# Optimization experiments

Hardware: AMD Instinct MI355X
Metric: run time of the kernel (lower is better)

The kernel has to match this reference:

```python
import jax, jax.numpy as jnp
import numpy as np

H = 1024        # hidden_size
F = 4096        # intermediate_size
E = 8           # num_local_experts
TOP_K = 2       # num_experts_per_tok
B, S = 1, 2048


def setup_inputs() -> dict:
    key = jax.random.key(0)
    k0, k1, k2, k3 = jax.random.split(key, 4)
    hidden_states = jax.random.normal(k0, (B, S, H), dtype=jnp.float32)
    # torch nn.Linear weights: gate [E_out, in]; experts stacked on leading axis
    gate_w = jax.random.normal(k1, (E, H), dtype=jnp.float32) * 0.02
    gate_up_w = jax.random.normal(k2, (E, 2 * F, H), dtype=jnp.float32) * 0.02
    down_w = jax.random.normal(k3, (E, H, F), dtype=jnp.float32) * 0.02
    return {"hidden_states": hidden_states, "gate_w": gate_w,
            "gate_up_w": gate_up_w, "down_w": down_w}


def reference(hidden_states, gate_w, gate_up_w, down_w):
    b, s, h = hidden_states.shape
    x = hidden_states.reshape(-1, h)                      # [T, H]
    # router: softmax in float32, top-k, renormalize
    router_logits = x @ gate_w.T                          # [T, E]
    probs = jax.nn.softmax(router_logits.astype(jnp.float32), axis=-1)
    topw, sel = jax.lax.top_k(probs, TOP_K)               # [T, K]
    topw = topw / jnp.sum(topw, axis=-1, keepdims=True)
    topw = topw.astype(x.dtype)
    # combine weights [T, E]: zero for unselected experts -> same math as
    # the per-expert gather/scatter loop (full capacity, no dropped tokens)
    combine = jnp.sum(jax.nn.one_hot(sel, E, dtype=x.dtype) * topw[..., None], axis=1)
    # all experts on all tokens (dense-equivalent of masked dispatch)
    gu = jnp.einsum('th,efh->etf', x, gate_up_w)          # [E, T, 2F]
    gate, up = gu[..., :F], gu[..., F:]
    hact = up * jax.nn.gelu(gate, approximate=False)      # [E, T, F]
    expert_out = jnp.einsum('etf,ehf->eth', hact, down_w) # [E, T, H]
    out = jnp.einsum('eth,te->th', expert_out, combine)   # [T, H]
    return out.reshape(b, s, h)
```

## Files before the change

### kernel.cpp

```cpp
#include <hip/hip_runtime.h>

#define Hdim 1024
#define Fdim 4096
#define NE   8
#define NT   2048
#define MT_MAX 16
#define KSPLIT 4

typedef __attribute__((ext_vector_type(8))) short short8;
typedef __attribute__((ext_vector_type(4))) short short4v;
typedef __attribute__((ext_vector_type(4))) float f32x4;

__device__ __forceinline__ unsigned short bf16r(float f) {
  union { float fv; unsigned u; } v; v.fv = f;
  unsigned u = v.u;
  return (unsigned short)((u + 0x7FFFu + ((u >> 16) & 1u)) >> 16);
}

__global__ void k_router(const float* __restrict__ x, const float* __restrict__ gw,
                         int* __restrict__ counts, int* __restrict__ sel,
                         float* __restrict__ selw) {
  int wave = threadIdx.x >> 6;
  int l    = threadIdx.x & 63;
  int t    = blockIdx.x * 4 + wave;
  const float* xp = x + (size_t)t * Hdim;
  float acc[NE];
#pragma unroll
  for (int e = 0; e < NE; e++) acc[e] = 0.f;
  for (int h = l; h < Hdim; h += 64) {
    float xv = xp[h];
#pragma unroll
    for (int e = 0; e < NE; e++) acc[e] += xv * gw[e * Hdim + h];
  }
#pragma unroll
  for (int e = 0; e < NE; e++) {
    float v = acc[e];
#pragma unroll
    for (int off = 32; off > 0; off >>= 1) v += __shfl_down(v, off, 64);
    acc[e] = v;
  }
  if (l == 0) {
    int b0 = 0; float v0 = acc[0];
    for (int e = 1; e < NE; e++) if (acc[e] > v0) { v0 = acc[e]; b0 = e; }
    int b1 = -1; float v1 = -1e30f;
    for (int e = 0; e < NE; e++) if (e != b0 && acc[e] > v1) { v1 = acc[e]; b1 = e; }
    float w0 = 1.f / (1.f + expf(v1 - v0));
    atomicAdd(&counts[b0], 1);
    atomicAdd(&counts[b1], 1);
    sel[2 * t]     = b0;
    sel[2 * t + 1] = b1;
    selw[2 * t]     = w0;
    selw[2 * t + 1] = 1.f - w0;
  }
}

__global__ void k_scatter(const int* __restrict__ counts, const int* __restrict__ sel,
                          const float* __restrict__ selw, int* __restrict__ offsets,
                          int* __restrict__ rowids, float* __restrict__ pairw) {
  __shared__ int soff[NE];
  __shared__ int scur[NE];
  if (threadIdx.x == 0) {
    int s = 0;
    for (int e = 0; e < NE; e++) { soff[e] = s; offsets[e] = s; s += counts[e]; scur[e] = 0; }
  }
  __syncthreads();
  for (int t = threadIdx.x; t < NT; t += blockDim.x) {
#pragma unroll
    for (int j = 0; j < 2; j++) {
      int e = sel[2 * t + j];
      int p = atomicAdd(&scur[e], 1);
      rowids[soff[e] + p] = t;
      pairw[soff[e] + p]  = selw[2 * t + j];
    }
  }
}

__global__ __launch_bounds__(256, 2)
void k_gate_up(const float* __restrict__ x, const float* __restrict__ gup,
               const int* __restrict__ counts, const int* __restrict__ offsets,
               const int* __restrict__ rowids, unsigned short* __restrict__ hact) {
  int e  = blockIdx.y >> 4;
  int mt = blockIdx.y & 15;
  int n  = counts[e];
  if (mt * 128 >= n) return;
  int base = offsets[e];
  int row0 = mt * 128;
  int f0   = blockIdx.x * 64;

  __shared__ __align__(16) unsigned short As[128][32];
  __shared__ __align__(16) unsigned short Bs[128][32];
  __shared__ int rid[128];

  int tid = threadIdx.x;
  if (tid < 128) {
    int r = row0 + tid;
    rid[tid] = (r < n) ? rowids[base + r] : rowids[base];
  }
  __syncthreads();

  int kc   = (tid & 7) * 4;
  int trow = tid >> 3;
  const float* ap[4];
  const float* bp[4];
#pragma unroll
  for (int p = 0; p < 4; p++) {
    int ar = p * 32 + trow;
    ap[p] = x + (size_t)rid[ar] * Hdim + kc;
    int f = (ar < 64) ? (f0 + ar) : (Fdim + f0 + (ar - 64));
    bp[p] = gup + ((size_t)e * 2 * Fdim + f) * Hdim + kc;
  }

  int wave = tid >> 6, lane = tid & 63;
  int wy = wave >> 1, wx = wave & 1;
  int lrow = lane & 15, lk = (lane >> 4) * 8;
  f32x4 acc[4][4] = {};

  float4 ra[4], rb[4];
#pragma unroll
  for (int p = 0; p < 4; p++) { ra[p] = *(const float4*)(ap[p]); rb[p] = *(const float4*)(bp[p]); }

  for (int k0 = 0; k0 < Hdim; k0 += 32) {
    __syncthreads();
#pragma unroll
    for (int p = 0; p < 4; p++) {
      int ar = p * 32 + trow;
      short4v sa;
      sa.x = (short)bf16r(ra[p].x); sa.y = (short)bf16r(ra[p].y);
      sa.z = (short)bf16r(ra[p].z); sa.w = (short)bf16r(ra[p].w);
      *(short4v*)&As[ar][kc] = sa;
      short4v sb;
      sb.x = (short)bf16r(rb[p].x); sb.y = (short)bf16r(rb[p].y);
      sb.z = (short)bf16r(rb[p].z); sb.w = (short)bf16r(rb[p].w);
      *(short4v*)&Bs[ar][kc] = sb;
    }
    if (k0 + 32 < Hdim) {
#pragma unroll
      for (int p = 0; p < 4; p++) {
        ra[p] = *(const float4*)(ap[p] + k0 + 32);
        rb[p] = *(const float4*)(bp[p] + k0 + 32);
      }
    }
    __syncthreads();
    short8 a[4], b[4];
#pragma unroll
    for (int i = 0; i < 4; i++) a[i] = *(const short8*)&As[wy * 64 + i * 16 + lrow][lk];
    b[0] = *(const short8*)&Bs[wx * 32 + lrow][lk];
    b[1] = *(const short8*)&Bs[wx * 32 + 16 + lrow][lk];
    b[2] = *(const short8*)&Bs[64 + wx * 32 + lrow][lk];
    b[3] = *(const short8*)&Bs[64 + wx * 32 + 16 + lrow][lk];
#pragma unroll
    for (int i = 0; i < 4; i++)
#pragma unroll
      for (int j = 0; j < 4; j++)
        acc[i][j] = __builtin_amdgcn_mfma_f32_16x16x32_bf16(a[i], b[j], acc[i][j], 0, 0, 0);
  }

  int quad = lane >> 4;
#pragma unroll
  for (int i = 0; i < 4; i++) {
#pragma unroll
    for (int r = 0; r < 4; r++) {
      int rl = row0 + wy * 64 + i * 16 + quad * 4 + r;
      if (rl < n) {
        size_t rowoff = (size_t)(base + rl) * Fdim + f0 + wx * 32;
#pragma unroll
        for (int j = 0; j < 2; j++) {
          float g = acc[i][j][r];
          float u = acc[i][j + 2][r];
          float ge = 0.5f * g * (1.f + erff(g * 0.70710678118654752f));
          hact[rowoff + j * 16 + lrow] = bf16r(u * ge);
        }
      }
    }
  }
}

__global__ __launch_bounds__(256, 2)
void k_down(const unsigned short* __restrict__ hact, const float* __restrict__ dw,
            const int* __restrict__ counts, const int* __restrict__ offsets,
            const int* __restrict__ rowids, const float* __restrict__ pairw,
            float* __restrict__ out) {
  int e  = blockIdx.y >> 4;
  int mt = blockIdx.y & 15;
  int n  = counts[e];
  if (mt * 128 >= n) return;
  int base = offsets[e];
  int row0 = mt * 128;
  int h0   = blockIdx.x * 128;
  int kbeg = blockIdx.z * (Fdim / KSPLIT);
  int kend = kbeg + Fdim / KSPLIT;

  __shared__ __align__(16) unsigned short As[128][32];
  __shared__ __align__(16) unsigned short Bs[128][32];

  int tid = threadIdx.x;
  int wave = tid >> 6, lane = tid & 63;
  int wy = wave >> 1, wx = wave & 1;
  int lrow = lane & 15, lk = (lane >> 4) * 8;

  const unsigned short* asrc[2];
#pragma unroll
  for (int p = 0; p < 2; p++) {
    int idx = p * 256 + tid;
    int row = idx >> 2, seg = idx & 3;
    int slot = base + row0 + row;
    if (slot > NT * 2 - 1) slot = NT * 2 - 1;
    asrc[p] = hact + (size_t)slot * Fdim + seg * 8;
  }
  int kc   = (tid & 7) * 4;
  int trow = tid >> 3;
  const float* bp[4];
#pragma unroll
  for (int p = 0; p < 4; p++) {
    int j = p * 32 + trow;
    bp[p] = dw + ((size_t)e * Hdim + h0 + j) * Fdim + kc;
  }

  int4   raw[2];
  float4 rbw[4];
#pragma unroll
  for (int p = 0; p < 2; p++) raw[p] = *(const int4*)(asrc[p] + kbeg);
#pragma unroll
  for (int p = 0; p < 4; p++) rbw[p] = *(const float4*)(bp[p] + kbeg);

  f32x4 acc[4][4] = {};
  for (int k0 = kbeg; k0 < kend; k0 += 32) {
    __syncthreads();
#pragma unroll
    for (int p = 0; p < 2; p++) {
      int idx = p * 256 + tid;
      int row = idx >> 2, seg = idx & 3;
      *(int4*)&As[row][seg * 8] = raw[p];
    }
#pragma unroll
    for (int p = 0; p < 4; p++) {
      int j = p * 32 + trow;
      short4v sb;
      sb.x = (short)bf16r(rbw[p].x); sb.y = (short)bf16r(rbw[p].y);
      sb.z = (short)bf16r(rbw[p].z); sb.w = (short)bf16r(rbw[p].w);
      *(short4v*)&Bs[j][kc] = sb;
    }
    if (k0 + 32 < kend) {
#pragma unroll
      for (int p = 0; p < 2; p++) raw[p] = *(const int4*)(asrc[p] + k0 + 32);
#pragma unroll
      for (int p = 0; p < 4; p++) rbw[p] = *(const float4*)(bp[p] + k0 + 32);
    }
    __syncthreads();
    short8 a[4], b[4];
#pragma unroll
    for (int i = 0; i < 4; i++) a[i] = *(const short8*)&As[wy * 64 + i * 16 + lrow][lk];
#pragma unroll
    for (int j = 0; j < 4; j++) b[j] = *(const short8*)&Bs[wx * 64 + j * 16 + lrow][lk];
#pragma unroll
    for (int i = 0; i < 4; i++)
#pragma unroll
      for (int j = 0; j < 4; j++)
        acc[i][j] = __builtin_amdgcn_mfma_f32_16x16x32_bf16(a[i], b[j], acc[i][j], 0, 0, 0);
  }

  int quad = lane >> 4;
#pragma unroll
  for (int i = 0; i < 4; i++) {
#pragma unroll
    for (int r = 0; r < 4; r++) {
      int rl = row0 + wy * 64 + i * 16 + quad * 4 + r;
      if (rl < n) {
        int slot = base + rl;
        int t    = rowids[slot];
        float wv = pairw[slot];
        float* op = out + (size_t)t * Hdim + h0 + wx * 64;
#pragma unroll
        for (int j = 0; j < 4; j++)
          atomicAdd(op + j * 16 + lrow, wv * acc[i][j][r]);
      }
    }
  }
}

extern "C" void kernel_launch(void* const* d_in, const int* in_sizes, int n_in,
                              void* d_out, int out_size, void* d_ws, size_t ws_size,
                              hipStream_t stream) {
  const float* x   = (const float*)d_in[0];
  const float* gw  = (const float*)d_in[1];
  const float* gup = (const float*)d_in[2];
  const float* dwn = (const float*)d_in[3];
  float* out = (float*)d_out;

  char* ws = (char*)d_ws;
  int*   counts  = (int*)(ws + 0);
  int*   offsets = (int*)(ws + 128);
  int*   sel     = (int*)(ws + 4096);
  float* selw    = (float*)(ws + 4096 + 16384);
  int*   rowids  = (int*)(ws + 4096 + 32768);
  float* pairw   = (float*)(ws + 4096 + 49152);
  unsigned short* hact = (unsigned short*)(ws + (1 << 20));

  hipMemsetAsync(ws, 0, 4096, stream);
  hipMemsetAsync(d_out, 0, (size_t)out_size * sizeof(float), stream);

  k_router<<<NT / 4, 256, 0, stream>>>(x, gw, counts, sel, selw);
  k_scatter<<<1, 1024, 0, stream>>>(counts, sel, selw, offsets, rowids, pairw);
  k_gate_up<<<dim3(Fdim / 64, NE * MT_MAX), 256, 0, stream>>>(x, gup, counts, offsets, rowids, hact);
  k_down<<<dim3(Hdim / 128, NE * MT_MAX, KSPLIT), 256, 0, stream>>>(hact, dwn, counts, offsets, rowids, pairw, out);
}
```

Baseline: 779.0 us.

## Replace atomic down-proj accumulation with split-K partials and a combine kernel

The down-projection kernel now writes weighted partial results per K-split into a workspace buffer instead of doing float atomicAdd into the output. A new combine kernel sums the two experts' partials for each token, using a token-to-slot map built during scatter. The output memset goes away. Separately, KSPLIT drops from 4 to 2 and the down kernel's K tile widens to 64. Shared-memory rows in both GEMM kernels get padding to reduce LDS bank conflicts. The trade-off is an extra 32MB partial buffer write and read plus one more launch, while removing atomic contention and making the reduction order deterministic.

```diff
diff --git a/kernel.cpp b/kernel.cpp
--- a/kernel.cpp
+++ b/kernel.cpp
@@ -5,7 +5,7 @@
 #define NE   8
 #define NT   2048
 #define MT_MAX 16
-#define KSPLIT 4
+#define KSPLIT 2
 
 typedef __attribute__((ext_vector_type(8))) short short8;
 typedef __attribute__((ext_vector_type(4))) short short4v;
@@ -56,7 +56,8 @@
 
 __global__ void k_scatter(const int* __restrict__ counts, const int* __restrict__ sel,
                           const float* __restrict__ selw, int* __restrict__ offsets,
-                          int* __restrict__ rowids, float* __restrict__ pairw) {
+                          int* __restrict__ rowids, float* __restrict__ pairw,
+                          int* __restrict__ tok2slot) {
   __shared__ int soff[NE];
   __shared__ int scur[NE];
   if (threadIdx.x == 0) {
@@ -69,8 +70,10 @@
     for (int j = 0; j < 2; j++) {
       int e = sel[2 * t + j];
       int p = atomicAdd(&scur[e], 1);
-      rowids[soff[e] + p] = t;
-      pairw[soff[e] + p]  = selw[2 * t + j];
+      int slot = soff[e] + p;
+      rowids[slot]        = t;
+      pairw[slot]         = selw[2 * t + j];
+      tok2slot[2 * t + j] = slot;
     }
   }
 }
@@ -87,8 +90,8 @@
   int row0 = mt * 128;
   int f0   = blockIdx.x * 64;
 
-  __shared__ __align__(16) unsigned short As[128][32];
-  __shared__ __align__(16) unsigned short Bs[128][32];
+  __shared__ __align__(16) unsigned short As[128][40];
+  __shared__ __align__(16) unsigned short Bs[128][40];
   __shared__ int rid[128];
 
   int tid = threadIdx.x;
@@ -179,7 +182,7 @@
 void k_down(const unsigned short* __restrict__ hact, const float* __restrict__ dw,
             const int* __restrict__ counts, const int* __restrict__ offsets,
             const int* __restrict__ rowids, const float* __restrict__ pairw,
-            float* __restrict__ out) {
+            float* __restrict__ part) {
   int e  = blockIdx.y >> 4;
   int mt = blockIdx.y & 15;
   int n  = counts[e];
@@ -187,76 +190,80 @@
   int base = offsets[e];
   int row0 = mt * 128;
   int h0   = blockIdx.x * 128;
-  int kbeg = blockIdx.z * (Fdim / KSPLIT);
-  int kend = kbeg + Fdim / KSPLIT;
-
-  __shared__ __align__(16) unsigned short As[128][32];
-  __shared__ __align__(16) unsigned short Bs[128][32];
+  const int KC = Fdim / KSPLIT;
+  int kbeg = blockIdx.z * KC;
+  int kend = kbeg + KC;
+
+  __shared__ __align__(16) unsigned short As[128][72];
+  __shared__ __align__(16) unsigned short Bs[128][72];
 
   int tid = threadIdx.x;
   int wave = tid >> 6, lane = tid & 63;
   int wy = wave >> 1, wx = wave & 1;
-  int lrow = lane & 15, lk = (lane >> 4) * 8;
-
-  const unsigned short* asrc[2];
-#pragma unroll
-  for (int p = 0; p < 2; p++) {
+  int lrow = lane & 15, lkq = (lane >> 4) * 8;
+
+  const unsigned short* asrc[4];
+#pragma unroll
+  for (int p = 0; p < 4; p++) {
     int idx = p * 256 + tid;
-    int row = idx >> 2, seg = idx & 3;
+    int row = idx >> 3, seg = idx & 7;
     int slot = base + row0 + row;
     if (slot > NT * 2 - 1) slot = NT * 2 - 1;
     asrc[p] = hact + (size_t)slot * Fdim + seg * 8;
   }
-  int kc   = (tid & 7) * 4;
-  int trow = tid >> 3;
-  const float* bp[4];
-#pragma unroll
-  for (int p = 0; p < 4; p++) {
-    int j = p * 32 + trow;
-    bp[p] = dw + ((size_t)e * Hdim + h0 + j) * Fdim + kc;
-  }
-
-  int4   raw[2];
-  float4 rbw[4];
-#pragma unroll
-  for (int p = 0; p < 2; p++) raw[p] = *(const int4*)(asrc[p] + kbeg);
-#pragma unroll
-  for (int p = 0; p < 4; p++) rbw[p] = *(const float4*)(bp[p] + kbeg);
+  const float* bsrc[8];
+#pragma unroll
+  for (int p = 0; p < 8; p++) {
+    int idx = p * 256 + tid;
+    int row = idx >> 4, seg = idx & 15;
+    bsrc[p] = dw + ((size_t)e * Hdim + h0 + row) * Fdim + seg * 4;
+  }
+
+  int4   raw[4];
+  float4 rbw[8];
+#pragma unroll
+  for (int p = 0; p < 4; p++) raw[p] = *(const int4*)(asrc[p] + kbeg);
+#pragma unroll
+  for (int p = 0; p < 8; p++) rbw[p] = *(const float4*)(bsrc[p] + kbeg);
 
   f32x4 acc[4][4] = {};
-  for (int k0 = kbeg; k0 < kend; k0 += 32) {
+  for (int k0 = kbeg; k0 < kend; k0 += 64) {
     __syncthreads();
 #pragma unroll
-    for (int p = 0; p < 2; p++) {
+    for (int p = 0; p < 4; p++) {
       int idx = p * 256 + tid;
-      int row = idx >> 2, seg = idx & 3;
+      int row = idx >> 3, seg = idx & 7;
       *(int4*)&As[row][seg * 8] = raw[p];
     }
 #pragma unroll
-    for (int p = 0; p < 4; p++) {
-      int j = p * 32 + trow;
+    for (int p = 0; p < 8; p++) {
+      int idx = p * 256 + tid;
+      int row = idx >> 4, seg = idx & 15;
       short4v sb;
       sb.x = (short)bf16r(rbw[p].x); sb.y = (short)bf16r(rbw[p].y);
       sb.z = (short)bf16r(rbw[p].z); sb.w = (short)bf16r(rbw[p].w);
-      *(short4v*)&Bs[j][kc] = sb;
-    }
-    if (k0 + 32 < kend) {
-#pragma unroll
-      for (int p = 0; p < 2; p++) raw[p] = *(const int4*)(asrc[p] + k0 + 32);
-#pragma unroll
-      for (int p = 0; p < 4; p++) rbw[p] = *(const float4*)(bp[p] + k0 + 32);
+      *(short4v*)&Bs[row][seg * 4] = sb;
+    }
+    if (k0 + 64 < kend) {
+#pragma unroll
+      for (int p = 0; p < 4; p++) raw[p] = *(const int4*)(asrc[p] + k0 + 64);
+#pragma unroll
+      for (int p = 0; p < 8; p++) rbw[p] = *(const float4*)(bsrc[p] + k0 + 64);
     }
     __syncthreads();
-    short8 a[4], b[4];
-#pragma unroll
-    for (int i = 0; i < 4; i++) a[i] = *(const short8*)&As[wy * 64 + i * 16 + lrow][lk];
-#pragma unroll
-    for (int j = 0; j < 4; j++) b[j] = *(const short8*)&Bs[wx * 64 + j * 16 + lrow][lk];
-#pragma unroll
-    for (int i = 0; i < 4; i++)
-#pragma unroll
-      for (int j = 0; j < 4; j++)
-        acc[i][j] = __builtin_amdgcn_mfma_f32_16x16x32_bf16(a[i], b[j], acc[i][j], 0, 0, 0);
+#pragma unroll
+    for (int ks = 0; ks < 2; ks++) {
+      short8 a[4], b[4];
+#pragma unroll
+      for (int i = 0; i < 4; i++) a[i] = *(const short8*)&As[wy * 64 + i * 16 + lrow][ks * 32 + lkq];
+#pragma unroll
+      for (int j = 0; j < 4; j++) b[j] = *(const short8*)&Bs[wx * 64 + j * 16 + lrow][ks * 32 + lkq];
+#pragma unroll
+      for (int i = 0; i < 4; i++)
+#pragma unroll
+        for (int j = 0; j < 4; j++)
+          acc[i][j] = __builtin_amdgcn_mfma_f32_16x16x32_bf16(a[i], b[j], acc[i][j], 0, 0, 0);
+    }
   }
 
   int quad = lane >> 4;
@@ -267,15 +274,34 @@
       int rl = row0 + wy * 64 + i * 16 + quad * 4 + r;
       if (rl < n) {
         int slot = base + rl;
-        int t    = rowids[slot];
         float wv = pairw[slot];
-        float* op = out + (size_t)t * Hdim + h0 + wx * 64;
+        float* op = part + ((size_t)blockIdx.z * (NT * 2) + slot) * Hdim + h0 + wx * 64;
 #pragma unroll
         for (int j = 0; j < 4; j++)
-          atomicAdd(op + j * 16 + lrow, wv * acc[i][j][r]);
+          op[j * 16 + lrow] = wv * acc[i][j][r];
       }
     }
   }
+}
+
+__global__ __launch_bounds__(256)
+void k_combine(const float* __restrict__ part, const int* __restrict__ tok2slot,
+               float* __restrict__ out) {
+  int idx = blockIdx.x * 256 + threadIdx.x;
+  int t  = idx >> 8;
+  int hc = (idx & 255) << 2;
+  int s0 = tok2slot[2 * t];
+  int s1 = tok2slot[2 * t + 1];
+  float4 a = *(const float4*)&part[(size_t)s0 * Hdim + hc];
+  float4 b = *(const float4*)&part[((size_t)(NT * 2) + s0) * Hdim + hc];
+  float4 c = *(const float4*)&part[(size_t)s1 * Hdim + hc];
+  float4 d = *(const float4*)&part[((size_t)(NT * 2) + s1) * Hdim + hc];
+  float4 s;
+  s.x = (a.x + b.x) + (c.x + d.x);
+  s.y = (a.y + b.y) + (c.y + d.y);
+  s.z = (a.z + b.z) + (c.z + d.z);
+  s.w = (a.w + b.w) + (c.w + d.w);
+  *(float4*)&out[(size_t)t * Hdim + hc] = s;
 }
 
 extern "C" void kernel_launch(void* const* d_in, const int* in_sizes, int n_in,
@@ -288,19 +314,21 @@
   float* out = (float*)d_out;
 
   char* ws = (char*)d_ws;
-  int*   counts  = (int*)(ws + 0);
-  int*   offsets = (int*)(ws + 128);
-  int*   sel     = (int*)(ws + 4096);
-  float* selw    = (float*)(ws + 4096 + 16384);
-  int*   rowids  = (int*)(ws + 4096 + 32768);
-  float* pairw   = (float*)(ws + 4096 + 49152);
+  int*   counts   = (int*)(ws + 0);
+  int*   offsets  = (int*)(ws + 128);
+  int*   sel      = (int*)(ws + 4096);
+  float* selw     = (float*)(ws + 4096 + 16384);
+  int*   rowids   = (int*)(ws + 4096 + 32768);
+  float* pairw    = (float*)(ws + 4096 + 49152);
+  int*   tok2slot = (int*)(ws + 4096 + 65536);
   unsigned short* hact = (unsigned short*)(ws + (1 << 20));
+  float* part = (float*)(ws + (1 << 20) + ((size_t)32 << 20));
 
   hipMemsetAsync(ws, 0, 4096, stream);
-  hipMemsetAsync(d_out, 0, (size_t)out_size * sizeof(float), stream);
 
   k_router<<<NT / 4, 256, 0, stream>>>(x, gw, counts, sel, selw);
-  k_scatter<<<1, 1024, 0, stream>>>(counts, sel, selw, offsets, rowids, pairw);
+  k_scatter<<<1, 1024, 0, stream>>>(counts, sel, selw, offsets, rowids, pairw, tok2slot);
   k_gate_up<<<dim3(Fdim / 64, NE * MT_MAX), 256, 0, stream>>>(x, gup, counts, offsets, rowids, hact);
-  k_down<<<dim3(Hdim / 128, NE * MT_MAX, KSPLIT), 256, 0, stream>>>(hact, dwn, counts, offsets, rowids, pairw, out);
-}
+  k_down<<<dim3(Hdim / 128, NE * MT_MAX, KSPLIT), 256, 0, stream>>>(hact, dwn, counts, offsets, rowids, pairw, part);
+  k_combine<<<NT * Hdim / 4 / 256, 256, 0, stream>>>(part, tok2slot, out);
+}
```

Measured after the change: 761.4 us. 2.3% less time.
